# Performance work log

Hardware: AMD Instinct MI355X
Metric: run time of the kernel (lower is better)

Reference implementation:

```python
import jax, jax.numpy as jnp
import numpy as np

G = 2048            # number of graphs in batch
NPG = 128           # nodes per graph (fixed, implied by Linear(128*hid, 1))
IN_C = 151
HID = 64
N = G * NPG
E = 2_097_152       # intra-graph edges, avg degree 8
NEG_SLOPE = 0.2


def setup_inputs() -> dict:
    key = jax.random.key(0)
    ks = jax.random.split(key, 8)
    x = jax.random.normal(ks[0], (N, IN_C), dtype=jnp.float32)
    # intra-graph random edges: pick a graph, then src/dst within it
    g = jax.random.randint(ks[1], (E,), 0, G)
    src = g * NPG + jax.random.randint(ks[2], (E,), 0, NPG)
    dst = g * NPG + jax.random.randint(ks[3], (E,), 0, NPG)
    edge_index = jnp.stack([src, dst]).astype(jnp.int32)   # [2, E]
    W1 = jax.random.normal(ks[4], (IN_C, HID), jnp.float32) / np.sqrt(IN_C)
    att_src = jax.random.normal(ks[5], (HID,), jnp.float32) * 0.1
    att_dst = jax.random.normal(ks[6], (HID,), jnp.float32) * 0.1
    b1 = jnp.zeros((HID,), jnp.float32)
    Wlin = jax.random.normal(ks[7], (NPG * HID, 1), jnp.float32) / np.sqrt(NPG * HID)
    blin = jnp.zeros((1,), jnp.float32)
    return {"x": x, "edge_index": edge_index, "W1": W1, "att_src": att_src,
            "att_dst": att_dst, "b1": b1, "Wlin": Wlin, "blin": blin}


def gat_conv(x, edge_index, W, a_src, a_dst, b):
    """PyG GATConv, heads=1, concat=True, add_self_loops=True."""
    n = x.shape[0]
    h = x @ W                                   # [N, HID] transformed features
    loops = jnp.arange(n, dtype=edge_index.dtype)
    src = jnp.concatenate([edge_index[0], loops])
    dst = jnp.concatenate([edge_index[1], loops])
    # edge score: a_src . h[j] + a_dst . h[i], j->i
    alpha = (h @ a_src)[src] + (h @ a_dst)[dst]            # [E+N]
    alpha = jax.nn.leaky_relu(alpha, NEG_SLOPE)
    # segment softmax over incoming edges of each target node
    amax = jax.ops.segment_max(alpha, dst, num_segments=n)
    ex = jnp.exp(alpha - amax[dst])
    denom = jax.ops.segment_sum(ex, dst, num_segments=n)
    w = ex / denom[dst]                                    # [E+N]
    out = jax.ops.segment_sum(h[src] * w[:, None], dst, num_segments=n)
    return out + b


def reference(x, edge_index, W1, att_src, att_dst, b1, Wlin, blin):
    h = jax.nn.relu(gat_conv(x, edge_index, W1, att_src, att_dst, b1))  # [N, HID]
    h = h.reshape(G, NPG * HID)        # linearize(x, batch): 128 nodes/graph
    logits = h @ Wlin + blin           # [G, 1]
    return jax.nn.sigmoid(logits)
```

## Files before the change

### kernel.cpp

```cpp
#include <hip/hip_runtime.h>
#include <hip/hip_bf16.h>

#define G_ 2048
#define NPG_ 128
#define INC_ 151
#define HID_ 64
#define NNODES_ (G_ * NPG_)
#define NEDGES_ 2097152

typedef __hip_bfloat16 bf16;
typedef short bf16x8v __attribute__((ext_vector_type(8)));
typedef float f32x4 __attribute__((ext_vector_type(4)));

static __device__ __forceinline__ short f2bs(float f) {
    __hip_bfloat16 b = __float2bfloat16(f);
    return __builtin_bit_cast(short, b);
}

__global__ void __launch_bounds__(256) k0C1(const float* __restrict__ W1,
                                            bf16* __restrict__ Bt,
                                            const int* __restrict__ ei,
                                            unsigned int* __restrict__ bccount) {
    __shared__ unsigned int hist[256];
    const int tid = threadIdx.x;
    if (blockIdx.x >= 256) {
        int i = (blockIdx.x - 256) * 256 + tid;
        if (i < 64 * 168) {
            int n = i / 168, k = i - n * 168;
            float v = (k < 151) ? W1[k * 64 + n] : 0.f;
            Bt[i] = __float2bfloat16(v);
        }
        return;
    }
    hist[tid] = 0;
    __syncthreads();
    const int e0 = blockIdx.x * 8192;
    for (int e = e0 + tid; e < e0 + 8192; e += 256)
        atomicAdd(&hist[ei[e] >> 10], 1u);
    __syncthreads();
    bccount[blockIdx.x * 256 + tid] = hist[tid];
}

__global__ void __launch_bounds__(256) kC2a(unsigned int* __restrict__ bccount,
                                            unsigned int* __restrict__ totals) {
    __shared__ unsigned int sc[256];
    const int tid = threadIdx.x, bk = blockIdx.x;
    unsigned int c = bccount[tid * 256 + bk];
    sc[tid] = c;
    __syncthreads();
    for (int off = 1; off < 256; off <<= 1) {
        unsigned int v = (tid >= off) ? sc[tid - off] : 0;
        __syncthreads();
        sc[tid] += v;
        __syncthreads();
    }
    bccount[tid * 256 + bk] = sc[tid] - c;
    if (tid == 255) totals[bk] = sc[255];
}

__global__ void __launch_bounds__(256) kC2b(const unsigned int* __restrict__ totals,
                                            unsigned int* __restrict__ cbase,
                                            unsigned int* __restrict__ base8) {
    __shared__ unsigned int sc[256];
    const int tid = threadIdx.x;
    unsigned int c = totals[tid];
    sc[tid] = c;
    __syncthreads();
    for (int off = 1; off < 256; off <<= 1) {
        unsigned int v = (tid >= off) ? sc[tid - off] : 0;
        __syncthreads();
        sc[tid] += v;
        __syncthreads();
    }
    cbase[tid] = sc[tid] - c;
    if (tid == 255) {
        cbase[256] = sc[255];
        base8[G_ * 8] = NEDGES_;
    }
}

__global__ void __launch_bounds__(256) kC3_scatter(const int* __restrict__ ei,
                                                   const unsigned int* __restrict__ bccount,
                                                   const unsigned int* __restrict__ cbase,
                                                   unsigned int* __restrict__ rbuf) {
    __shared__ unsigned int cur[256];
    const int tid = threadIdx.x;
    cur[tid] = cbase[tid] + bccount[blockIdx.x * 256 + tid];
    __syncthreads();
    const int e0 = blockIdx.x * 8192;
    for (int e = e0 + tid; e < e0 + 8192; e += 256) {
        int s = ei[e];
        int d = ei[NEDGES_ + e];
        int bk = s >> 10;
        unsigned int pos = atomicAdd(&cur[bk], 1u);
        rbuf[pos] = (((unsigned int)s & 1023u) << 7) | ((unsigned int)d & 127u);
    }
}

__global__ void __launch_bounds__(256) kC4_fine(const unsigned int* __restrict__ rbuf,
                                                const unsigned int* __restrict__ cbase,
                                                unsigned int* __restrict__ base8,
                                                unsigned short* __restrict__ eb) {
    __shared__ unsigned int lcnt[64];
    __shared__ unsigned int cur[64];
    const int tid = threadIdx.x;
    const int b = blockIdx.x;
    const unsigned int s0 = cbase[b], s1 = cbase[b + 1];
    if (tid < 64) lcnt[tid] = 0;
    __syncthreads();
    for (unsigned int i = s0 + tid; i < s1; i += 256) {
        unsigned int rec = rbuf[i];
        int key = ((rec >> 11) & 0x38) | ((rec >> 4) & 7);
        atomicAdd(&lcnt[key], 1u);
    }
    __syncthreads();
    if (tid == 0) {
        unsigned int r = 0;
#pragma unroll
        for (int j = 0; j < 64; j++) {
            base8[b * 64 + j] = s0 + r;
            cur[j] = s0 + r;
            r += lcnt[j];
        }
    }
    __syncthreads();
    const int lane = tid & 63;
    for (unsigned int i = s0 + tid; i < s1; i += 256) {
        unsigned int rec = rbuf[i];
        int key = ((rec >> 11) & 0x38) | ((rec >> 4) & 7);
        unsigned long long m = __ballot(1);
#pragma unroll
        for (int bit = 0; bit < 6; bit++) {
            unsigned long long bb = __ballot((key >> bit) & 1);
            m &= ((key >> bit) & 1) ? bb : ~bb;
        }
        int leader = __builtin_ctzll(m);
        int rank = __builtin_popcountll(m & ((1ull << lane) - 1ull));
        unsigned int bp = 0;
        if (lane == leader)
            bp = atomicAdd(&cur[key], (unsigned int)__builtin_popcountll(m));
        bp = __shfl((int)bp, leader);
        eb[bp + rank] = (unsigned short)(rec & 0x3FFFu);
    }
}

__global__ void __launch_bounds__(256) k3_graph(
        const float* __restrict__ x, const bf16* __restrict__ Bt,
        const float* __restrict__ att_src, const float* __restrict__ att_dst,
        const unsigned short* __restrict__ eb, const unsigned int* __restrict__ base8,
        const float* __restrict__ b1, const float* __restrict__ Wlin,
        const float* __restrict__ blin, float* __restrict__ out) {
    __shared__ __align__(16) unsigned char lds[61952];
    short* Bs = (short*)lds;
    short* Xs = (short*)(lds + 21504);
    short* Ab = (short*)lds;
    float* S = (float*)(lds + 34816);
    short* hT = (short*)(lds + 43008);
    float* asL = (float*)(lds + 60416);
    float* adL = (float*)(lds + 60928);
    float* dinv = (float*)(lds + 61440);

    const int tid = threadIdx.x;
    const int g = blockIdx.x;
    const int w = tid >> 6, lane = tid & 63;
    const int quad = lane >> 4, m = lane & 15;

    {
        const uint4* bsrc = (const uint4*)Bt;
        uint4* bdst = (uint4*)Bs;
        for (int i = tid; i < 1344; i += 256) bdst[i] = bsrc[i];
    }
    float as4[4], ad4[4];
#pragma unroll
    for (int t = 0; t < 4; t++) {
        as4[t] = att_src[t * 16 + m];
        ad4[t] = att_dst[t * 16 + m];
    }

#pragma unroll 1
    for (int half = 0; half < 2; half++) {
        for (int i = tid; i < 576; i += 256) {
            int r = i / 9, c = 151 + (i - (i / 9) * 9);
            Xs[r * 168 + c] = 0;
        }
        const float4* xsrc = (const float4*)(x + ((size_t)g * 128 + half * 64) * 151);
        for (int i = tid; i < 2416; i += 256) {
            float4 v = xsrc[i];
            unsigned gi = 4u * (unsigned)i;
            unsigned r = gi / 151u;
            unsigned c = gi - r * 151u;
            float vv[4] = {v.x, v.y, v.z, v.w};
#pragma unroll
            for (int j = 0; j < 4; j++) {
                Xs[r * 168 + c] = f2bs(vv[j]);
                if (++c == 151u) { c = 0u; ++r; }
            }
        }
        __syncthreads();

        f32x4 acc[4];
#pragma unroll
        for (int t = 0; t < 4; t++) acc[t] = (f32x4){0.f, 0.f, 0.f, 0.f};
        const int xrow = w * 16 + m;
#pragma unroll
        for (int ks = 0; ks < 5; ks++) {
            const int k0 = ks * 32 + quad * 8;
            bf16x8v af = *(const bf16x8v*)&Xs[xrow * 168 + k0];
#pragma unroll
            for (int t = 0; t < 4; t++) {
                bf16x8v bfr = *(const bf16x8v*)&Bs[(t * 16 + m) * 168 + k0];
                acc[t] = __builtin_amdgcn_mfma_f32_16x16x32_bf16(af, bfr, acc[t], 0, 0, 0);
            }
        }
        const int node0 = half * 64 + w * 16 + quad * 4;
#pragma unroll
        for (int r = 0; r < 4; r++) {
            float s = acc[0][r] * as4[0] + acc[1][r] * as4[1] +
                      acc[2][r] * as4[2] + acc[3][r] * as4[3];
            float d = acc[0][r] * ad4[0] + acc[1][r] * ad4[1] +
                      acc[2][r] * ad4[2] + acc[3][r] * ad4[3];
#pragma unroll
            for (int off = 1; off <= 8; off <<= 1) {
                s += __shfl_xor(s, off);
                d += __shfl_xor(d, off);
            }
            if (m == 0) { asL[node0 + r] = s; adL[node0 + r] = d; }
        }
#pragma unroll
        for (int t = 0; t < 4; t++) {
            const int col = t * 16 + m;
            unsigned int u01 = ((unsigned int)(unsigned short)f2bs(acc[t][1]) << 16) |
                               (unsigned short)f2bs(acc[t][0]);
            unsigned int u23 = ((unsigned int)(unsigned short)f2bs(acc[t][3]) << 16) |
                               (unsigned short)f2bs(acc[t][2]);
            *(unsigned int*)&hT[col * 136 + node0] = u01;
            *(unsigned int*)&hT[col * 136 + node0 + 2] = u23;
        }
        __syncthreads();
    }

#pragma unroll 1
    for (int p = 0; p < 8; p++) {
        for (int i = tid; i < 512; i += 256)
            ((float4*)S)[i] = make_float4(0.f, 0.f, 0.f, 0.f);
        __syncthreads();
        if (tid < 16) {
            int node = 16 * p + tid;
            float a = asL[node] + adL[node];
            a = (a > 0.f) ? a : 0.2f * a;
            atomicAdd(&S[(tid << 7) + node], __expf(a));
        }
        const unsigned int q0 = base8[(g << 3) + p];
        const unsigned int q1 = base8[(g << 3) + p + 1];
        for (unsigned int k = q0 + tid; k < q1; k += 256) {
            unsigned int v = eb[k];
            int sl = v >> 7, dl = v & 127;
            float a = asL[sl] + adL[dl];
            a = (a > 0.f) ? a : 0.2f * a;
            atomicAdd(&S[((dl & 15) << 7) + sl], __expf(a));
        }
        __syncthreads();
        {
            int r = tid >> 4;
            int col = (tid & 15) << 3;
            float4 v0 = ((const float4*)S)[tid * 2];
            float4 v1 = ((const float4*)S)[tid * 2 + 1];
            float rs = v0.x + v0.y + v0.z + v0.w + v1.x + v1.y + v1.z + v1.w;
            bf16x8v pk = {f2bs(v0.x), f2bs(v0.y), f2bs(v0.z), f2bs(v0.w),
                          f2bs(v1.x), f2bs(v1.y), f2bs(v1.z), f2bs(v1.w)};
            *(bf16x8v*)&Ab[(16 * p + r) * 136 + col] = pk;
#pragma unroll
            for (int off = 1; off <= 8; off <<= 1) rs += __shfl_xor(rs, off);
            if ((tid & 15) == 0) dinv[16 * p + r] = 1.f / rs;
        }
        __syncthreads();
    }

    const int i0 = w * 32;
    f32x4 acc[2][4];
#pragma unroll
    for (int mt = 0; mt < 2; mt++)
#pragma unroll
        for (int nt = 0; nt < 4; nt++) acc[mt][nt] = (f32x4){0.f, 0.f, 0.f, 0.f};

#pragma unroll
    for (int ks = 0; ks < 4; ks++) {
        const int k0 = ks * 32 + quad * 8;
        bf16x8v a0 = *(const bf16x8v*)&Ab[(i0 + m) * 136 + k0];
        bf16x8v a1 = *(const bf16x8v*)&Ab[(i0 + 16 + m) * 136 + k0];
#pragma unroll
        for (int nt = 0; nt < 4; nt++) {
            bf16x8v bfr = *(const bf16x8v*)&hT[(nt * 16 + m) * 136 + k0];
            acc[0][nt] = __builtin_amdgcn_mfma_f32_16x16x32_bf16(a0, bfr, acc[0][nt], 0, 0, 0);
            acc[1][nt] = __builtin_amdgcn_mfma_f32_16x16x32_bf16(a1, bfr, acc[1][nt], 0, 0, 0);
        }
    }

    float dv[2][4];
#pragma unroll
    for (int mt = 0; mt < 2; mt++)
#pragma unroll
        for (int r = 0; r < 4; r++)
            dv[mt][r] = dinv[i0 + mt * 16 + quad * 4 + r];

    float pacc = 0.f;
#pragma unroll
    for (int nt = 0; nt < 4; nt++) {
        float bb = b1[nt * 16 + m];
#pragma unroll
        for (int mt = 0; mt < 2; mt++) {
#pragma unroll
            for (int r = 0; r < 4; r++) {
                int il = i0 + mt * 16 + quad * 4 + r;
                float v = acc[mt][nt][r] * dv[mt][r] + bb;
                v = v > 0.f ? v : 0.f;
                pacc += v * Wlin[il * 64 + nt * 16 + m];
            }
        }
    }
#pragma unroll
    for (int off = 32; off; off >>= 1) pacc += __shfl_xor(pacc, off);

    __syncthreads();
    if (lane == 0) S[w] = pacc;
    __syncthreads();
    if (tid == 0) {
        float logit = S[0] + S[1] + S[2] + S[3] + blin[0];
        out[g] = 1.f / (1.f + __expf(-logit));
    }
}

extern "C" void kernel_launch(void* const* d_in, const int* in_sizes, int n_in,
                              void* d_out, int out_size, void* d_ws, size_t ws_size,
                              hipStream_t stream) {
    (void)in_sizes; (void)n_in; (void)out_size; (void)ws_size;
    const float* x       = (const float*)d_in[0];
    const int*   ei      = (const int*)d_in[1];
    const float* W1      = (const float*)d_in[2];
    const float* att_src = (const float*)d_in[3];
    const float* att_dst = (const float*)d_in[4];
    const float* b1      = (const float*)d_in[5];
    const float* Wlin    = (const float*)d_in[6];
    const float* blin    = (const float*)d_in[7];
    float* out = (float*)d_out;

    char* ws = (char*)d_ws;
    bf16*           Bt      = (bf16*)ws;
    unsigned int*   bccount = (unsigned int*)(ws + 65536);
    unsigned int*   cbase   = (unsigned int*)(ws + 327680);
    unsigned int*   totals  = (unsigned int*)(ws + 331776);
    unsigned int*   base8   = (unsigned int*)(ws + 335872);
    unsigned int*   rbuf    = (unsigned int*)(ws + 405504);
    unsigned short* eb      = (unsigned short*)(ws + 8794112);

    k0C1<<<298, 256, 0, stream>>>(W1, Bt, ei, bccount);
    kC2a<<<256, 256, 0, stream>>>(bccount, totals);
    kC2b<<<1, 256, 0, stream>>>(totals, cbase, base8);
    kC3_scatter<<<256, 256, 0, stream>>>(ei, bccount, cbase, rbuf);
    kC4_fine<<<256, 256, 0, stream>>>(rbuf, cbase, base8, eb);
    k3_graph<<<G_, 256, 0, stream>>>(x, Bt, att_src, att_dst, eb, base8,
                                     b1, Wlin, blin, out);
}
```

Baseline: 381.2 us.

## Fold prefix-scan kernels into scatter and fine sort, widen graph kernel to 512 threads

The two scan kernels are removed. Each scatter and fine-sort block now recomputes the column prefix sums from the raw block counts, which cuts two launches at the cost of redundant reads of the count matrix. The per-graph kernel moves from 256 to 512 threads and loads all 128 nodes' features in one pass instead of two halves. The padded K stride drops from 168 to 160 and LDS grows to about 80KB. Each of the eight waves now handles 16 output rows, which raises parallelism per graph but may reduce how many blocks fit on a CU.

```diff
diff --git a/kernel.cpp b/kernel.cpp
--- a/kernel.cpp
+++ b/kernel.cpp
@@ -25,11 +25,9 @@
     const int tid = threadIdx.x;
     if (blockIdx.x >= 256) {
         int i = (blockIdx.x - 256) * 256 + tid;
-        if (i < 64 * 168) {
-            int n = i / 168, k = i - n * 168;
-            float v = (k < 151) ? W1[k * 64 + n] : 0.f;
-            Bt[i] = __float2bfloat16(v);
-        }
+        int n = i / 160, k = i - n * 160;
+        float v = (k < 151) ? W1[k * 64 + n] : 0.f;
+        Bt[i] = __float2bfloat16(v);
         return;
     }
     hist[tid] = 0;
@@ -41,12 +39,20 @@
     bccount[blockIdx.x * 256 + tid] = hist[tid];
 }
 
-__global__ void __launch_bounds__(256) kC2a(unsigned int* __restrict__ bccount,
-                                            unsigned int* __restrict__ totals) {
+__global__ void __launch_bounds__(256) kC3_scatter(const int* __restrict__ ei,
+                                                   const unsigned int* __restrict__ bccount,
+                                                   unsigned int* __restrict__ rbuf) {
     __shared__ unsigned int sc[256];
-    const int tid = threadIdx.x, bk = blockIdx.x;
-    unsigned int c = bccount[tid * 256 + bk];
-    sc[tid] = c;
+    __shared__ unsigned int cur[256];
+    const int tid = threadIdx.x;
+    const int j = blockIdx.x;
+    unsigned int part = 0, tot = 0;
+    for (int i = 0; i < 256; i++) {
+        unsigned int c = bccount[i * 256 + tid];
+        if (i < j) part += c;
+        tot += c;
+    }
+    sc[tid] = tot;
     __syncthreads();
     for (int off = 1; off < 256; off <<= 1) {
         unsigned int v = (tid >= off) ? sc[tid - off] : 0;
@@ -54,40 +60,9 @@
         sc[tid] += v;
         __syncthreads();
     }
-    bccount[tid * 256 + bk] = sc[tid] - c;
-    if (tid == 255) totals[bk] = sc[255];
-}
-
-__global__ void __launch_bounds__(256) kC2b(const unsigned int* __restrict__ totals,
-                                            unsigned int* __restrict__ cbase,
-                                            unsigned int* __restrict__ base8) {
-    __shared__ unsigned int sc[256];
-    const int tid = threadIdx.x;
-    unsigned int c = totals[tid];
-    sc[tid] = c;
-    __syncthreads();
-    for (int off = 1; off < 256; off <<= 1) {
-        unsigned int v = (tid >= off) ? sc[tid - off] : 0;
-        __syncthreads();
-        sc[tid] += v;
-        __syncthreads();
-    }
-    cbase[tid] = sc[tid] - c;
-    if (tid == 255) {
-        cbase[256] = sc[255];
-        base8[G_ * 8] = NEDGES_;
-    }
-}
-
-__global__ void __launch_bounds__(256) kC3_scatter(const int* __restrict__ ei,
-                                                   const unsigned int* __restrict__ bccount,
-                                                   const unsigned int* __restrict__ cbase,
-                                                   unsigned int* __restrict__ rbuf) {
-    __shared__ unsigned int cur[256];
-    const int tid = threadIdx.x;
-    cur[tid] = cbase[tid] + bccount[blockIdx.x * 256 + tid];
-    __syncthreads();
-    const int e0 = blockIdx.x * 8192;
+    cur[tid] = (sc[tid] - tot) + part;
+    __syncthreads();
+    const int e0 = j * 8192;
     for (int e = e0 + tid; e < e0 + 8192; e += 256) {
         int s = ei[e];
         int d = ei[NEDGES_ + e];
@@ -98,16 +73,27 @@
 }
 
 __global__ void __launch_bounds__(256) kC4_fine(const unsigned int* __restrict__ rbuf,
-                                                const unsigned int* __restrict__ cbase,
+                                                const unsigned int* __restrict__ bccount,
                                                 unsigned int* __restrict__ base8,
                                                 unsigned short* __restrict__ eb) {
+    __shared__ unsigned int sc[256];
     __shared__ unsigned int lcnt[64];
     __shared__ unsigned int cur[64];
     const int tid = threadIdx.x;
     const int b = blockIdx.x;
-    const unsigned int s0 = cbase[b], s1 = cbase[b + 1];
+    unsigned int tot = 0;
+    for (int i = 0; i < 256; i++) tot += bccount[i * 256 + tid];
+    sc[tid] = tot;
     if (tid < 64) lcnt[tid] = 0;
     __syncthreads();
+    for (int off = 1; off < 256; off <<= 1) {
+        unsigned int v = (tid >= off) ? sc[tid - off] : 0;
+        __syncthreads();
+        sc[tid] += v;
+        __syncthreads();
+    }
+    const unsigned int s0 = (b > 0) ? sc[b - 1] : 0;
+    const unsigned int s1 = sc[b];
     for (unsigned int i = s0 + tid; i < s1; i += 256) {
         unsigned int rec = rbuf[i];
         int key = ((rec >> 11) & 0x38) | ((rec >> 4) & 7);
@@ -122,6 +108,7 @@
             cur[j] = s0 + r;
             r += lcnt[j];
         }
+        if (b == 255) base8[G_ * 8] = NEDGES_;
     }
     __syncthreads();
     const int lane = tid & 63;
@@ -144,21 +131,21 @@
     }
 }
 
-__global__ void __launch_bounds__(256) k3_graph(
+__global__ void __launch_bounds__(512, 4) k3_graph(
         const float* __restrict__ x, const bf16* __restrict__ Bt,
         const float* __restrict__ att_src, const float* __restrict__ att_dst,
         const unsigned short* __restrict__ eb, const unsigned int* __restrict__ base8,
         const float* __restrict__ b1, const float* __restrict__ Wlin,
         const float* __restrict__ blin, float* __restrict__ out) {
-    __shared__ __align__(16) unsigned char lds[61952];
-    short* Bs = (short*)lds;
-    short* Xs = (short*)(lds + 21504);
+    __shared__ __align__(16) unsigned char lds[80384];
+    short* Xs = (short*)lds;
+    short* Bs = (short*)(lds + 40960);
     short* Ab = (short*)lds;
     float* S = (float*)(lds + 34816);
-    short* hT = (short*)(lds + 43008);
-    float* asL = (float*)(lds + 60416);
-    float* adL = (float*)(lds + 60928);
-    float* dinv = (float*)(lds + 61440);
+    short* hT = (short*)(lds + 61440);
+    float* asL = (float*)(lds + 78848);
+    float* adL = (float*)(lds + 79360);
+    float* dinv = (float*)(lds + 79872);
 
     const int tid = threadIdx.x;
     const int g = blockIdx.x;
@@ -168,23 +155,15 @@
     {
         const uint4* bsrc = (const uint4*)Bt;
         uint4* bdst = (uint4*)Bs;
-        for (int i = tid; i < 1344; i += 256) bdst[i] = bsrc[i];
-    }
-    float as4[4], ad4[4];
-#pragma unroll
-    for (int t = 0; t < 4; t++) {
-        as4[t] = att_src[t * 16 + m];
-        ad4[t] = att_dst[t * 16 + m];
-    }
-
-#pragma unroll 1
-    for (int half = 0; half < 2; half++) {
-        for (int i = tid; i < 576; i += 256) {
-            int r = i / 9, c = 151 + (i - (i / 9) * 9);
-            Xs[r * 168 + c] = 0;
-        }
-        const float4* xsrc = (const float4*)(x + ((size_t)g * 128 + half * 64) * 151);
-        for (int i = tid; i < 2416; i += 256) {
+        for (int i = tid; i < 1280; i += 512) bdst[i] = bsrc[i];
+    }
+    for (int i = tid; i < 1152; i += 512) {
+        int r = i / 9, c = 151 + (i - (i / 9) * 9);
+        Xs[r * 160 + c] = 0;
+    }
+    {
+        const float4* xsrc = (const float4*)(x + (size_t)g * 128 * 151);
+        for (int i = tid; i < 4832; i += 512) {
             float4 v = xsrc[i];
             unsigned gi = 4u * (unsigned)i;
             unsigned r = gi / 151u;
@@ -192,12 +171,20 @@
             float vv[4] = {v.x, v.y, v.z, v.w};
 #pragma unroll
             for (int j = 0; j < 4; j++) {
-                Xs[r * 168 + c] = f2bs(vv[j]);
+                Xs[r * 160 + c] = f2bs(vv[j]);
                 if (++c == 151u) { c = 0u; ++r; }
             }
         }
-        __syncthreads();
-
+    }
+    float as4[4], ad4[4];
+#pragma unroll
+    for (int t = 0; t < 4; t++) {
+        as4[t] = att_src[t * 16 + m];
+        ad4[t] = att_dst[t * 16 + m];
+    }
+    __syncthreads();
+
+    {
         f32x4 acc[4];
 #pragma unroll
         for (int t = 0; t < 4; t++) acc[t] = (f32x4){0.f, 0.f, 0.f, 0.f};
@@ -205,14 +192,14 @@
 #pragma unroll
         for (int ks = 0; ks < 5; ks++) {
             const int k0 = ks * 32 + quad * 8;
-            bf16x8v af = *(const bf16x8v*)&Xs[xrow * 168 + k0];
+            bf16x8v af = *(const bf16x8v*)&Xs[xrow * 160 + k0];
 #pragma unroll
             for (int t = 0; t < 4; t++) {
-                bf16x8v bfr = *(const bf16x8v*)&Bs[(t * 16 + m) * 168 + k0];
+                bf16x8v bfr = *(const bf16x8v*)&Bs[(t * 16 + m) * 160 + k0];
                 acc[t] = __builtin_amdgcn_mfma_f32_16x16x32_bf16(af, bfr, acc[t], 0, 0, 0);
             }
         }
-        const int node0 = half * 64 + w * 16 + quad * 4;
+        const int node0 = w * 16 + quad * 4;
 #pragma unroll
         for (int r = 0; r < 4; r++) {
             float s = acc[0][r] * as4[0] + acc[1][r] * as4[1] +
@@ -236,13 +223,12 @@
             *(unsigned int*)&hT[col * 136 + node0] = u01;
             *(unsigned int*)&hT[col * 136 + node0 + 2] = u23;
         }
-        __syncthreads();
-    }
+    }
+    __syncthreads();
 
 #pragma unroll 1
     for (int p = 0; p < 8; p++) {
-        for (int i = tid; i < 512; i += 256)
-            ((float4*)S)[i] = make_float4(0.f, 0.f, 0.f, 0.f);
+        ((float4*)S)[tid] = make_float4(0.f, 0.f, 0.f, 0.f);
         __syncthreads();
         if (tid < 16) {
             int node = 16 * p + tid;
@@ -252,7 +238,7 @@
         }
         const unsigned int q0 = base8[(g << 3) + p];
         const unsigned int q1 = base8[(g << 3) + p + 1];
-        for (unsigned int k = q0 + tid; k < q1; k += 256) {
+        for (unsigned int k = q0 + tid; k < q1; k += 512) {
             unsigned int v = eb[k];
             int sl = v >> 7, dl = v & 127;
             float a = asL[sl] + adL[dl];
@@ -261,61 +247,53 @@
         }
         __syncthreads();
         {
-            int r = tid >> 4;
-            int col = (tid & 15) << 3;
-            float4 v0 = ((const float4*)S)[tid * 2];
-            float4 v1 = ((const float4*)S)[tid * 2 + 1];
-            float rs = v0.x + v0.y + v0.z + v0.w + v1.x + v1.y + v1.z + v1.w;
-            bf16x8v pk = {f2bs(v0.x), f2bs(v0.y), f2bs(v0.z), f2bs(v0.w),
-                          f2bs(v1.x), f2bs(v1.y), f2bs(v1.z), f2bs(v1.w)};
-            *(bf16x8v*)&Ab[(16 * p + r) * 136 + col] = pk;
-#pragma unroll
-            for (int off = 1; off <= 8; off <<= 1) rs += __shfl_xor(rs, off);
-            if ((tid & 15) == 0) dinv[16 * p + r] = 1.f / rs;
-        }
-        __syncthreads();
-    }
-
-    const int i0 = w * 32;
-    f32x4 acc[2][4];
-#pragma unroll
-    for (int mt = 0; mt < 2; mt++)
-#pragma unroll
-        for (int nt = 0; nt < 4; nt++) acc[mt][nt] = (f32x4){0.f, 0.f, 0.f, 0.f};
+            int r = tid >> 5;
+            int col = (tid & 31) << 2;
+            float4 v = ((const float4*)S)[tid];
+            float rs = v.x + v.y + v.z + v.w;
+            unsigned int u01 = ((unsigned int)(unsigned short)f2bs(v.y) << 16) |
+                               (unsigned short)f2bs(v.x);
+            unsigned int u23 = ((unsigned int)(unsigned short)f2bs(v.w) << 16) |
+                               (unsigned short)f2bs(v.z);
+            uint2 pk = make_uint2(u01, u23);
+            *(uint2*)&Ab[(16 * p + r) * 136 + col] = pk;
+#pragma unroll
+            for (int off = 1; off <= 16; off <<= 1) rs += __shfl_xor(rs, off);
+            if ((tid & 31) == 0) dinv[16 * p + r] = 1.f / rs;
+        }
+        __syncthreads();
+    }
+
+    const int i0 = w * 16;
+    f32x4 acc[4];
+#pragma unroll
+    for (int nt = 0; nt < 4; nt++) acc[nt] = (f32x4){0.f, 0.f, 0.f, 0.f};
 
 #pragma unroll
     for (int ks = 0; ks < 4; ks++) {
         const int k0 = ks * 32 + quad * 8;
         bf16x8v a0 = *(const bf16x8v*)&Ab[(i0 + m) * 136 + k0];
-        bf16x8v a1 = *(const bf16x8v*)&Ab[(i0 + 16 + m) * 136 + k0];
 #pragma unroll
         for (int nt = 0; nt < 4; nt++) {
             bf16x8v bfr = *(const bf16x8v*)&hT[(nt * 16 + m) * 136 + k0];
-            acc[0][nt] = __builtin_amdgcn_mfma_f32_16x16x32_bf16(a0, bfr, acc[0][nt], 0, 0, 0);
-            acc[1][nt] = __builtin_amdgcn_mfma_f32_16x16x32_bf16(a1, bfr, acc[1][nt], 0, 0, 0);
-        }
-    }
-
-    float dv[2][4];
-#pragma unroll
-    for (int mt = 0; mt < 2; mt++)
-#pragma unroll
-        for (int r = 0; r < 4; r++)
-            dv[mt][r] = dinv[i0 + mt * 16 + quad * 4 + r];
+            acc[nt] = __builtin_amdgcn_mfma_f32_16x16x32_bf16(a0, bfr, acc[nt], 0, 0, 0);
+        }
+    }
+
+    float dv[4];
+#pragma unroll
+    for (int r = 0; r < 4; r++) dv[r] = dinv[i0 + quad * 4 + r];
 
     float pacc = 0.f;
 #pragma unroll
     for (int nt = 0; nt < 4; nt++) {
         float bb = b1[nt * 16 + m];
 #pragma unroll
-        for (int mt = 0; mt < 2; mt++) {
-#pragma unroll
-            for (int r = 0; r < 4; r++) {
-                int il = i0 + mt * 16 + quad * 4 + r;
-                float v = acc[mt][nt][r] * dv[mt][r] + bb;
-                v = v > 0.f ? v : 0.f;
-                pacc += v * Wlin[il * 64 + nt * 16 + m];
-            }
+        for (int r = 0; r < 4; r++) {
+            int il = i0 + quad * 4 + r;
+            float v = acc[nt][r] * dv[r] + bb;
+            v = v > 0.f ? v : 0.f;
+            pacc += v * Wlin[il * 64 + nt * 16 + m];
         }
     }
 #pragma unroll
@@ -325,7 +303,8 @@
     if (lane == 0) S[w] = pacc;
     __syncthreads();
     if (tid == 0) {
-        float logit = S[0] + S[1] + S[2] + S[3] + blin[0];
+        float logit = S[0] + S[1] + S[2] + S[3] +
+                      S[4] + S[5] + S[6] + S[7] + blin[0];
         out[g] = 1.f / (1.f + __expf(-logit));
     }
 }
@@ -347,17 +326,13 @@
     char* ws = (char*)d_ws;
     bf16*           Bt      = (bf16*)ws;
     unsigned int*   bccount = (unsigned int*)(ws + 65536);
-    unsigned int*   cbase   = (unsigned int*)(ws + 327680);
-    unsigned int*   totals  = (unsigned int*)(ws + 331776);
-    unsigned int*   base8   = (unsigned int*)(ws + 335872);
-    unsigned int*   rbuf    = (unsigned int*)(ws + 405504);
-    unsigned short* eb      = (unsigned short*)(ws + 8794112);
-
-    k0C1<<<298, 256, 0, stream>>>(W1, Bt, ei, bccount);
-    kC2a<<<256, 256, 0, stream>>>(bccount, totals);
-    kC2b<<<1, 256, 0, stream>>>(totals, cbase, base8);
-    kC3_scatter<<<256, 256, 0, stream>>>(ei, bccount, cbase, rbuf);
-    kC4_fine<<<256, 256, 0, stream>>>(rbuf, cbase, base8, eb);
-    k3_graph<<<G_, 256, 0, stream>>>(x, Bt, att_src, att_dst, eb, base8,
+    unsigned int*   base8   = (unsigned int*)(ws + 327680);
+    unsigned int*   rbuf    = (unsigned int*)(ws + 397312);
+    unsigned short* eb      = (unsigned short*)(ws + 8785920);
+
+    k0C1<<<296, 256, 0, stream>>>(W1, Bt, ei, bccount);
+    kC3_scatter<<<256, 256, 0, stream>>>(ei, bccount, rbuf);
+    kC4_fine<<<256, 256, 0, stream>>>(rbuf, bccount, base8, eb);
+    k3_graph<<<G_, 512, 0, stream>>>(x, Bt, att_src, att_dst, eb, base8,
                                      b1, Wlin, blin, out);
 }
```

New measurement: 366.2 us. 1.04x faster.
